# Kernel optimization log

Hardware: AMD Instinct MI355X
Metric: run time of the kernel (lower is better)

The kernel has to match this reference:

```python
import jax, jax.numpy as jnp
import numpy as np

BN_EPS = 1e-5

def _conv(x, W, b, stride, pad):
    # x: [B,C,H,W], W: [O,I,kh,kw]
    y = jax.lax.conv_general_dilated(
        x, W, window_strides=(stride, stride),
        padding=[(pad, pad), (pad, pad)],
        dimension_numbers=('NCHW', 'OIHW', 'NCHW'))
    return y + b[None, :, None, None]

def _bn(x, gamma, beta, mean, var):
    inv = gamma * jax.lax.rsqrt(var + BN_EPS)
    return x * inv[None, :, None, None] + (beta - mean * inv)[None, :, None, None]

def _haar_cD(x):
    # pywt.dwt2(x, 'haar') diagonal detail over last two axes (even H,W):
    # cD[i,j] = (x[2i,2j] - x[2i,2j+1] - x[2i+1,2j] + x[2i+1,2j+1]) / 2
    a = x[..., 0::2, 0::2]
    b = x[..., 0::2, 1::2]
    c = x[..., 1::2, 0::2]
    d = x[..., 1::2, 1::2]
    return (a - b - c + d) * 0.5

def setup_inputs() -> dict:
    key = jax.random.key(0)
    ks = jax.random.split(key, 20)
    B = 8192
    f32 = jnp.float32
    inp = {
        'x':   jax.random.normal(ks[0], (B, 3, 32, 32), dtype=f32),
        # conv1: 3 -> 32, k5 s2 p2
        'w1':  jax.random.normal(ks[1], (32, 3, 5, 5), dtype=f32) * 0.05,
        'b1':  jnp.zeros((32,), f32),
        'g1':  jnp.ones((32,), f32),
        'be1': jnp.zeros((32,), f32),
        'm1':  jax.random.normal(ks[2], (32,), dtype=f32) * 0.1,
        'v1':  jax.random.uniform(ks[3], (32,), dtype=f32, minval=0.5, maxval=1.5),
        # conv2: 32 -> 64, k3 s2 p1
        'w2':  jax.random.normal(ks[4], (64, 32, 3, 3), dtype=f32) * 0.05,
        'b2':  jnp.zeros((64,), f32),
        'g2':  jnp.ones((64,), f32),
        'be2': jnp.zeros((64,), f32),
        'm2':  jax.random.normal(ks[5], (64,), dtype=f32) * 0.1,
        'v2':  jax.random.uniform(ks[6], (64,), dtype=f32, minval=0.5, maxval=1.5),
        # attention conv: 64 -> 1, k1
        'wa':  jax.random.normal(ks[7], (1, 64, 1, 1), dtype=f32) * 0.1,
        'ba':  jnp.zeros((1,), f32),
        # decoder linears (torch Linear layout: [out, in])
        'wd1': jax.random.normal(ks[8], (512, 64 * 8 * 8), dtype=f32) * 0.02,
        'bd1': jnp.zeros((512,), f32),
        'wd2': jax.random.normal(ks[9], (128, 512), dtype=f32) * 0.04,
        'bd2': jnp.zeros((128,), f32),
    }
    return inp

def reference(x, w1, b1, g1, be1, m1, v1, w2, b2, g2, be2, m2, v2,
              wa, ba, wd1, bd1, wd2, bd2):
    # wavelet_conv stem
    h = jax.nn.relu(_bn(_conv(x, w1, b1, 2, 2), g1, be1, m1, v1))   # [B,32,16,16]
    feat = jax.nn.relu(_bn(_conv(h, w2, b2, 2, 1), g2, be2, m2, v2))  # [B,64,8,8]
    # Haar DWT diagonal-detail gate (detached in the original)
    cD = jax.lax.stop_gradient(_haar_cD(feat))                        # [B,64,4,4]
    cD_up = jnp.repeat(jnp.repeat(cD, 2, axis=-2), 2, axis=-1)        # [B,64,8,8]
    feat = feat * cD_up
    # attention gate
    attn = jax.nn.sigmoid(_conv(feat, wa, ba, 1, 0))                  # [B,1,8,8]
    feat = feat * attn
    # decode
    f = feat.reshape(feat.shape[0], -1)                               # [B,4096]
    h1 = jax.nn.relu(f @ wd1.T + bd1)                                  # [B,512]
    return jax.nn.sigmoid(h1 @ wd2.T + bd2)                            # [B,128]
```

## Files before the change

kernel.cpp:

```cpp
#include <hip/hip_runtime.h>
#include <hip/hip_bf16.h>

typedef __bf16 bf16x8 __attribute__((ext_vector_type(8)));
typedef __bf16 bf16x4 __attribute__((ext_vector_type(4)));
typedef float f32x4 __attribute__((ext_vector_type(4)));

#define BN_EPS 1e-5f

__device__ __forceinline__ void gl_lds16(const __bf16* g, __bf16* l) {
    __builtin_amdgcn_global_load_lds(
        (const __attribute__((address_space(1))) unsigned int*)g,
        (__attribute__((address_space(3))) unsigned int*)l,
        16, 0, 0);
}

__global__ __launch_bounds__(256) void wd1p_kernel(const float* __restrict__ wd1, __bf16* __restrict__ o) {
    __shared__ float t2[64][65];
    const int n = blockIdx.x;
    const int tid = threadIdx.x;
    const float* src = wd1 + (size_t)n * 4096;
    #pragma unroll
    for (int r = 0; r < 16; ++r) {
        int j = r * 256 + tid;
        t2[j & 63][j >> 6] = src[j];
    }
    __syncthreads();
    __bf16* dst = o + (size_t)n * 4096;
    #pragma unroll
    for (int r = 0; r < 16; ++r) {
        int t = r * 256 + tid;
        dst[t] = (__bf16)t2[t >> 6][t & 63];
    }
}

__global__ void prep_kernel(const float* __restrict__ wd2, const float* __restrict__ w1,
                            const float* __restrict__ w2,
                            __bf16* __restrict__ wd2o, __bf16* __restrict__ w1o,
                            __bf16* __restrict__ w2o) {
    int i = blockIdx.x * 256 + threadIdx.x;
    if (i < 65536) { wd2o[i] = (__bf16)wd2[i]; return; }
    i -= 65536;
    if (i < 4096) {
        int oc = i >> 7, rem = i & 127;
        int ot = rem >> 3, j = rem & 7;
        float v = 0.f;
        if (ot < 15 && j < 5) {
            int ic = ot / 5, ky = ot % 5;
            v = w1[((oc * 3 + ic) * 5 + ky) * 5 + j];
        }
        w1o[i] = (__bf16)v;
        return;
    }
    i -= 4096;
    if (i < 18432) {
        int oc = i / 288, rem = i % 288;
        int tap = rem / 32, ic = rem % 32;
        w2o[i] = (__bf16)w2[(oc * 32 + ic) * 9 + tap];
    }
}

__global__ __launch_bounds__(256, 5) void conv_fused_kernel(
    const float* __restrict__ x,
    const __bf16* __restrict__ w1r, const float* __restrict__ b1,
    const float* __restrict__ g1, const float* __restrict__ be1,
    const float* __restrict__ m1, const float* __restrict__ v1,
    const __bf16* __restrict__ w2r, const float* __restrict__ b2,
    const float* __restrict__ g2, const float* __restrict__ be2,
    const float* __restrict__ m2, const float* __restrict__ v2,
    const float* __restrict__ wa, const float* __restrict__ ba,
    __bf16* __restrict__ f)
{
    __shared__ __align__(16) __bf16 xsb[3 * 36 * 40];
    __shared__ __align__(16) char  ubuf[23120];
    __bf16* hsf  = (__bf16*)ubuf;
    float*  feat = (float*)ubuf;
    float*  cds  = (float*)(ubuf + 16384);
    float*  atn  = (float*)(ubuf + 20480);

    const int b    = blockIdx.x;
    const int tid  = threadIdx.x;
    const int lane = tid & 63;
    const int wave = tid >> 6;
    const int lo   = lane >> 4;
    const int ln   = lane & 15;

    {
        bf16x8 z = {};
        for (int i = tid; i < 540; i += 256) *(bf16x8*)&xsb[i * 8] = z;
        if (tid < 132) {
            int pi = tid >> 2, ch = tid & 3;
            int pix = (pi < 17) ? pi : (pi - 16) * 17;
            *(bf16x8*)&hsf[pix * 40 + ch * 8] = z;
        }
    }
    __syncthreads();

    {
        const float4* xb = (const float4*)(x + (size_t)b * 3072);
        #pragma unroll
        for (int r = 0; r < 3; ++r) {
            int c = r * 256 + tid;
            int plane = c >> 8, rem = c & 255;
            int row = rem >> 3, c4 = rem & 7;
            float4 v = xb[c];
            bf16x4 h;
            h[0] = (__bf16)v.x; h[1] = (__bf16)v.y; h[2] = (__bf16)v.z; h[3] = (__bf16)v.w;
            *(bf16x4*)&xsb[plane * 1440 + (row + 2) * 40 + 4 + c4 * 4] = h;
        }
    }

    bf16x8 bw1[2][4];
    #pragma unroll
    for (int nt = 0; nt < 2; ++nt)
        #pragma unroll
        for (int s = 0; s < 4; ++s)
            bw1[nt][s] = *(const bf16x8*)(w1r + (nt * 16 + ln) * 128 + (s * 4 + lo) * 8);
    __syncthreads();

    f32x4 c1[4][2] = {};
    const unsigned int* xw = (const unsigned int*)xsb;
    #pragma unroll
    for (int s = 0; s < 4; ++s) {
        const int o  = s * 4 + lo;
        const int ic = (o * 205) >> 10;
        const int ky = o - ic * 5;
        const bool dummy = (o == 15);
        const int icc = dummy ? 2 : ic;
        #pragma unroll
        for (int mt = 0; mt < 4; ++mt) {
            const int oy  = wave * 4 + mt;
            const int row = dummy ? 35 : (2 * oy + ky);
            const int dw  = icc * 720 + row * 20 + ln + 1;
            union { unsigned int u[4]; bf16x8 v; } fa;
            fa.u[0] = xw[dw]; fa.u[1] = xw[dw + 1]; fa.u[2] = xw[dw + 2]; fa.u[3] = 0;
            #pragma unroll
            for (int nt = 0; nt < 2; ++nt)
                c1[mt][nt] = __builtin_amdgcn_mfma_f32_16x16x32_bf16(fa.v, bw1[nt][s], c1[mt][nt], 0, 0, 0);
        }
    }

    #pragma unroll
    for (int nt = 0; nt < 2; ++nt) {
        const int oc  = nt * 16 + ln;
        const float inv = g1[oc] * rsqrtf(v1[oc] + BN_EPS);
        const float bb  = be1[oc] + (b1[oc] - m1[oc]) * inv;
        #pragma unroll
        for (int mt = 0; mt < 4; ++mt) {
            const int hy = wave * 4 + mt + 1;
            #pragma unroll
            for (int r = 0; r < 4; ++r) {
                const int hx = lo * 4 + r + 1;
                hsf[(hy * 17 + hx) * 40 + oc] = (__bf16)fmaxf(c1[mt][nt][r] * inv + bb, 0.f);
            }
        }
    }

    const int wm = wave >> 1, wn = wave & 1;
    bf16x8 bw2[2][9];
    #pragma unroll
    for (int nt = 0; nt < 2; ++nt) {
        const __bf16* wp = w2r + (wn * 32 + nt * 16 + ln) * 288 + lo * 8;
        #pragma unroll
        for (int ks = 0; ks < 9; ++ks)
            bw2[nt][ks] = *(const bf16x8*)(wp + ks * 32);
    }
    __syncthreads();

    f32x4 c2[2][2] = {};
    {
        int pixbase[2];
        #pragma unroll
        for (int mt = 0; mt < 2; ++mt) {
            int p = wm * 32 + mt * 16 + ln;
            int qy = p >> 3, qx = p & 7;
            pixbase[mt] = (2 * qy * 17 + 2 * qx) * 40 + lo * 8;
        }
        #pragma unroll
        for (int ks = 0; ks < 9; ++ks) {
            const int ty = ks / 3, tx = ks % 3;
            bf16x8 af[2];
            #pragma unroll
            for (int mt = 0; mt < 2; ++mt)
                af[mt] = *(const bf16x8*)&hsf[pixbase[mt] + (ty * 17 + tx) * 40];
            #pragma unroll
            for (int mt = 0; mt < 2; ++mt)
                #pragma unroll
                for (int nt = 0; nt < 2; ++nt)
                    c2[mt][nt] = __builtin_amdgcn_mfma_f32_16x16x32_bf16(af[mt], bw2[nt][ks], c2[mt][nt], 0, 0, 0);
        }
    }
    __syncthreads();

    #pragma unroll
    for (int nt = 0; nt < 2; ++nt) {
        const int oc  = wn * 32 + nt * 16 + ln;
        const float inv = g2[oc] * rsqrtf(v2[oc] + BN_EPS);
        const float bb  = be2[oc] + (b2[oc] - m2[oc]) * inv;
        #pragma unroll
        for (int mt = 0; mt < 2; ++mt)
            #pragma unroll
            for (int r = 0; r < 4; ++r) {
                const int p = wm * 32 + mt * 16 + lo * 4 + r;
                feat[oc * 64 + p] = fmaxf(c2[mt][nt][r] * inv + bb, 0.f);
            }
    }
    __syncthreads();

    #pragma unroll
    for (int r = 0; r < 4; ++r) {
        int idx = tid * 4 + r;
        int c = idx >> 4, yx = idx & 15;
        int y = yx >> 2, xx = yx & 3;
        float aa = feat[c * 64 + (2 * y) * 8 + 2 * xx];
        float bb = feat[c * 64 + (2 * y) * 8 + 2 * xx + 1];
        float cc = feat[c * 64 + (2 * y + 1) * 8 + 2 * xx];
        float dd = feat[c * 64 + (2 * y + 1) * 8 + 2 * xx + 1];
        cds[c * 16 + yx] = 0.5f * (aa - bb - cc + dd);
    }
    __syncthreads();

    const int q  = tid & 63;
    const int g  = wave;
    const int qy2 = q >> 3, qx2 = q & 7;
    const int qq = (qy2 >> 1) * 4 + (qx2 >> 1);
    float a2[16];
    float part = 0.f;
    #pragma unroll
    for (int j = 0; j < 16; ++j) {
        int oc = g * 16 + j;
        float v = feat[oc * 64 + q] * cds[oc * 16 + qq];
        a2[j] = v;
        part += v * wa[oc];
    }
    atn[g * 64 + q] = part;
    __syncthreads();
    float s2  = atn[q] + atn[64 + q] + atn[128 + q] + atn[192 + q] + ba[0];
    float sig = 1.f / (1.f + __expf(-s2));

    bf16x8 fo0, fo1;
    #pragma unroll
    for (int j = 0; j < 8; ++j) {
        fo0[j] = (__bf16)(a2[j] * sig);
        fo1[j] = (__bf16)(a2[j + 8] * sig);
    }
    __bf16* fb = f + (size_t)b * 4096 + q * 64 + g * 16;
    *(bf16x8*)fb = fo0;
    *(bf16x8*)(fb + 8) = fo1;
}

__global__ __launch_bounds__(256) void gemm1_kernel(
    const __bf16* __restrict__ A, const __bf16* __restrict__ B,
    const float* __restrict__ bias, __bf16* __restrict__ C)
{
    const int K = 4096, NOUT = 512;
    __shared__ __align__(16) __bf16 As[64][64];
    __shared__ __align__(16) __bf16 Bs[128][64];
    const int tid  = threadIdx.x;
    const int lane = tid & 63;
    const int wave = tid >> 6;
    const int lo = lane >> 4, ln = lane & 15;
    const int m0 = blockIdx.x * 64, n0 = blockIdx.y * 128;
    const int sw = ln & 7;
    f32x4 acc[4][2] = {};
    for (int k0 = 0; k0 < K; k0 += 64) {
        #pragma unroll
        for (int r = 0; r < 2; ++r) {
            int i = r * 256 + tid;
            int row = i >> 3, cs = i & 7;
            gl_lds16(A + (size_t)(m0 + row) * K + k0 + (cs ^ (row & 7)) * 8, &As[0][0] + i * 8);
        }
        #pragma unroll
        for (int r = 0; r < 4; ++r) {
            int i = r * 256 + tid;
            int row = i >> 3, cs = i & 7;
            gl_lds16(B + (size_t)(n0 + row) * K + k0 + (cs ^ (row & 7)) * 8, &Bs[0][0] + i * 8);
        }
        __syncthreads();
        #pragma unroll
        for (int s = 0; s < 2; ++s) {
            const int c = s * 4 + lo;
            const int slot = (c ^ sw) * 8;
            bf16x8 af[4], bfr[2];
            #pragma unroll
            for (int mt = 0; mt < 4; ++mt)
                af[mt] = *(const bf16x8*)(&As[mt * 16 + ln][slot]);
            #pragma unroll
            for (int nt = 0; nt < 2; ++nt)
                bfr[nt] = *(const bf16x8*)(&Bs[wave * 32 + nt * 16 + ln][slot]);
            #pragma unroll
            for (int mt = 0; mt < 4; ++mt)
                #pragma unroll
                for (int nt = 0; nt < 2; ++nt)
                    acc[mt][nt] = __builtin_amdgcn_mfma_f32_16x16x32_bf16(af[mt], bfr[nt], acc[mt][nt], 0, 0, 0);
        }
        __syncthreads();
    }
    #pragma unroll
    for (int mt = 0; mt < 4; ++mt)
        #pragma unroll
        for (int nt = 0; nt < 2; ++nt)
            #pragma unroll
            for (int r = 0; r < 4; ++r) {
                int m = m0 + mt * 16 + lo * 4 + r;
                int n = n0 + wave * 32 + nt * 16 + ln;
                float v = acc[mt][nt][r] + bias[n];
                C[(size_t)m * NOUT + n] = (__bf16)fmaxf(v, 0.f);
            }
}

__global__ __launch_bounds__(256) void gemm2_kernel(
    const __bf16* __restrict__ A, const __bf16* __restrict__ B,
    const float* __restrict__ bias, float* __restrict__ Out)
{
    const int K = 512, NOUT = 128;
    __shared__ __align__(16) __bf16 As[64][64];
    __shared__ __align__(16) __bf16 Bs[128][64];
    const int tid  = threadIdx.x;
    const int lane = tid & 63;
    const int wave = tid >> 6;
    const int lo = lane >> 4, ln = lane & 15;
    const int m0 = blockIdx.x * 64;
    const int sw = ln & 7;
    f32x4 acc[4][2] = {};
    for (int k0 = 0; k0 < K; k0 += 64) {
        #pragma unroll
        for (int r = 0; r < 2; ++r) {
            int i = r * 256 + tid;
            int row = i >> 3, cs = i & 7;
            gl_lds16(A + (size_t)(m0 + row) * K + k0 + (cs ^ (row & 7)) * 8, &As[0][0] + i * 8);
        }
        #pragma unroll
        for (int r = 0; r < 4; ++r) {
            int i = r * 256 + tid;
            int row = i >> 3, cs = i & 7;
            gl_lds16(B + (size_t)row * K + k0 + (cs ^ (row & 7)) * 8, &Bs[0][0] + i * 8);
        }
        __syncthreads();
        #pragma unroll
        for (int s = 0; s < 2; ++s) {
            const int c = s * 4 + lo;
            const int slot = (c ^ sw) * 8;
            bf16x8 af[4], bfr[2];
            #pragma unroll
            for (int mt = 0; mt < 4; ++mt)
                af[mt] = *(const bf16x8*)(&As[mt * 16 + ln][slot]);
            #pragma unroll
            for (int nt = 0; nt < 2; ++nt)
                bfr[nt] = *(const bf16x8*)(&Bs[wave * 32 + nt * 16 + ln][slot]);
            #pragma unroll
            for (int mt = 0; mt < 4; ++mt)
                #pragma unroll
                for (int nt = 0; nt < 2; ++nt)
                    acc[mt][nt] = __builtin_amdgcn_mfma_f32_16x16x32_bf16(af[mt], bfr[nt], acc[mt][nt], 0, 0, 0);
        }
        __syncthreads();
    }
    #pragma unroll
    for (int mt = 0; mt < 4; ++mt)
        #pragma unroll
        for (int nt = 0; nt < 2; ++nt)
            #pragma unroll
            for (int r = 0; r < 4; ++r) {
                int m = m0 + mt * 16 + lo * 4 + r;
                int n = wave * 32 + nt * 16 + ln;
                float v = acc[mt][nt][r] + bias[n];
                Out[(size_t)m * NOUT + n] = 1.f / (1.f + __expf(-v));
            }
}

extern "C" void kernel_launch(void* const* d_in, const int* in_sizes, int n_in,
                              void* d_out, int out_size, void* d_ws, size_t ws_size,
                              hipStream_t stream)
{
    const float* x   = (const float*)d_in[0];
    const float* w1  = (const float*)d_in[1];
    const float* b1  = (const float*)d_in[2];
    const float* g1  = (const float*)d_in[3];
    const float* be1 = (const float*)d_in[4];
    const float* m1  = (const float*)d_in[5];
    const float* v1  = (const float*)d_in[6];
    const float* w2  = (const float*)d_in[7];
    const float* b2  = (const float*)d_in[8];
    const float* g2  = (const float*)d_in[9];
    const float* be2 = (const float*)d_in[10];
    const float* m2  = (const float*)d_in[11];
    const float* v2  = (const float*)d_in[12];
    const float* wa  = (const float*)d_in[13];
    const float* ba  = (const float*)d_in[14];
    const float* wd1 = (const float*)d_in[15];
    const float* bd1 = (const float*)d_in[16];
    const float* wd2 = (const float*)d_in[17];
    const float* bd2 = (const float*)d_in[18];

    char* ws = (char*)d_ws;
    __bf16* f_bf   = (__bf16*)(ws);
    __bf16* h1_bf  = (__bf16*)(ws + 67108864);
    __bf16* wd1_bf = (__bf16*)(ws + 67108864 + 8388608);
    __bf16* wd2_bf = (__bf16*)(ws + 67108864 + 8388608 + 4194304);
    __bf16* w2r_bf = (__bf16*)(ws + 67108864 + 8388608 + 4194304 + 131072);
    __bf16* w1r_bf = (__bf16*)(ws + 67108864 + 8388608 + 4194304 + 131072 + 65536);

    prep_kernel<<<344, 256, 0, stream>>>(wd2, w1, w2, wd2_bf, w1r_bf, w2r_bf);
    wd1p_kernel<<<512, 256, 0, stream>>>(wd1, wd1_bf);

    conv_fused_kernel<<<8192, 256, 0, stream>>>(x, w1r_bf, b1, g1, be1, m1, v1,
                                                w2r_bf, b2, g2, be2, m2, v2, wa, ba, f_bf);

    dim3 g3(128, 4);
    gemm1_kernel<<<g3, 256, 0, stream>>>(f_bf, wd1_bf, bd1, h1_bf);

    gemm2_kernel<<<128, 256, 0, stream>>>(h1_bf, wd2_bf, bd2, (float*)d_out);
}
```

Measured before the change: 314.9 us.

## Transpose conv MFMA operands for vectorized epilogues; enlarge gemm1 tile to 128x128

The conv kernel swaps the MFMA operand order so each lane holds four consecutive output channels. That allows vectorized BN parameter loads, bf16x4 stores of conv1 output, and float4 stores of conv2 features into a new pixel-major, XOR-swizzled LDS layout, with matching vectorized reads in the Haar and attention stages. The aim is to cut scalar LDS traffic and bank conflicts. gemm1 now uses 128x128 tiles with a 2x2 wave layout and half as many M blocks. This raises reuse per block but doubles the accumulator registers and cuts the grid size.

```diff
diff --git a/kernel.cpp b/kernel.cpp
--- a/kernel.cpp
+++ b/kernel.cpp
@@ -57,6 +57,10 @@
         int tap = rem / 32, ic = rem % 32;
         w2o[i] = (__bf16)w2[(oc * 32 + ic) * 9 + tap];
     }
+}
+
+__device__ __forceinline__ int feat_addr(int p, int c) {
+    return p * 68 + ((((c >> 2) ^ ((p >> 3) & 3)) << 2) | (c & 3));
 }
 
 __global__ __launch_bounds__(256, 5) void conv_fused_kernel(
@@ -74,8 +78,8 @@
     __shared__ __align__(16) char  ubuf[23120];
     __bf16* hsf  = (__bf16*)ubuf;
     float*  feat = (float*)ubuf;
-    float*  cds  = (float*)(ubuf + 16384);
-    float*  atn  = (float*)(ubuf + 20480);
+    float*  cds  = (float*)(ubuf + 17408);
+    float*  atn  = (float*)(ubuf + 21760);
 
     const int b    = blockIdx.x;
     const int tid  = threadIdx.x;
@@ -111,10 +115,10 @@
 
     bf16x8 bw1[2][4];
     #pragma unroll
-    for (int nt = 0; nt < 2; ++nt)
+    for (int oct = 0; oct < 2; ++oct)
         #pragma unroll
         for (int s = 0; s < 4; ++s)
-            bw1[nt][s] = *(const bf16x8*)(w1r + (nt * 16 + ln) * 128 + (s * 4 + lo) * 8);
+            bw1[oct][s] = *(const bf16x8*)(w1r + (oct * 16 + ln) * 128 + (s * 4 + lo) * 8);
     __syncthreads();
 
     f32x4 c1[4][2] = {};
@@ -134,35 +138,44 @@
             union { unsigned int u[4]; bf16x8 v; } fa;
             fa.u[0] = xw[dw]; fa.u[1] = xw[dw + 1]; fa.u[2] = xw[dw + 2]; fa.u[3] = 0;
             #pragma unroll
-            for (int nt = 0; nt < 2; ++nt)
-                c1[mt][nt] = __builtin_amdgcn_mfma_f32_16x16x32_bf16(fa.v, bw1[nt][s], c1[mt][nt], 0, 0, 0);
-        }
-    }
-
-    #pragma unroll
-    for (int nt = 0; nt < 2; ++nt) {
-        const int oc  = nt * 16 + ln;
-        const float inv = g1[oc] * rsqrtf(v1[oc] + BN_EPS);
-        const float bb  = be1[oc] + (b1[oc] - m1[oc]) * inv;
+            for (int oct = 0; oct < 2; ++oct)
+                c1[mt][oct] = __builtin_amdgcn_mfma_f32_16x16x32_bf16(bw1[oct][s], fa.v, c1[mt][oct], 0, 0, 0);
+        }
+    }
+
+    #pragma unroll
+    for (int oct = 0; oct < 2; ++oct) {
+        const int ocb = oct * 16 + lo * 4;
+        const float4 gv = *(const float4*)(g1 + ocb);
+        const float4 vv = *(const float4*)(v1 + ocb);
+        const float4 bev = *(const float4*)(be1 + ocb);
+        const float4 b1v = *(const float4*)(b1 + ocb);
+        const float4 mv = *(const float4*)(m1 + ocb);
+        float inv[4], bb[4];
+        inv[0] = gv.x * rsqrtf(vv.x + BN_EPS); bb[0] = bev.x + (b1v.x - mv.x) * inv[0];
+        inv[1] = gv.y * rsqrtf(vv.y + BN_EPS); bb[1] = bev.y + (b1v.y - mv.y) * inv[1];
+        inv[2] = gv.z * rsqrtf(vv.z + BN_EPS); bb[2] = bev.z + (b1v.z - mv.z) * inv[2];
+        inv[3] = gv.w * rsqrtf(vv.w + BN_EPS); bb[3] = bev.w + (b1v.w - mv.w) * inv[3];
         #pragma unroll
         for (int mt = 0; mt < 4; ++mt) {
             const int hy = wave * 4 + mt + 1;
-            #pragma unroll
-            for (int r = 0; r < 4; ++r) {
-                const int hx = lo * 4 + r + 1;
-                hsf[(hy * 17 + hx) * 40 + oc] = (__bf16)fmaxf(c1[mt][nt][r] * inv + bb, 0.f);
-            }
+            const int hx = ln + 1;
+            bf16x4 hv;
+            #pragma unroll
+            for (int r = 0; r < 4; ++r)
+                hv[r] = (__bf16)fmaxf(c1[mt][oct][r] * inv[r] + bb[r], 0.f);
+            *(bf16x4*)&hsf[(hy * 17 + hx) * 40 + ocb] = hv;
         }
     }
 
     const int wm = wave >> 1, wn = wave & 1;
     bf16x8 bw2[2][9];
     #pragma unroll
-    for (int nt = 0; nt < 2; ++nt) {
-        const __bf16* wp = w2r + (wn * 32 + nt * 16 + ln) * 288 + lo * 8;
+    for (int oct = 0; oct < 2; ++oct) {
+        const __bf16* wp = w2r + (wn * 32 + oct * 16 + ln) * 288 + lo * 8;
         #pragma unroll
         for (int ks = 0; ks < 9; ++ks)
-            bw2[nt][ks] = *(const bf16x8*)(wp + ks * 32);
+            bw2[oct][ks] = *(const bf16x8*)(wp + ks * 32);
     }
     __syncthreads();
 
@@ -170,39 +183,50 @@
     {
         int pixbase[2];
         #pragma unroll
-        for (int mt = 0; mt < 2; ++mt) {
-            int p = wm * 32 + mt * 16 + ln;
+        for (int np = 0; np < 2; ++np) {
+            int p = wm * 32 + np * 16 + ln;
             int qy = p >> 3, qx = p & 7;
-            pixbase[mt] = (2 * qy * 17 + 2 * qx) * 40 + lo * 8;
+            pixbase[np] = (2 * qy * 17 + 2 * qx) * 40 + lo * 8;
         }
         #pragma unroll
         for (int ks = 0; ks < 9; ++ks) {
             const int ty = ks / 3, tx = ks % 3;
-            bf16x8 af[2];
-            #pragma unroll
-            for (int mt = 0; mt < 2; ++mt)
-                af[mt] = *(const bf16x8*)&hsf[pixbase[mt] + (ty * 17 + tx) * 40];
-            #pragma unroll
-            for (int mt = 0; mt < 2; ++mt)
+            bf16x8 bfp[2];
+            #pragma unroll
+            for (int np = 0; np < 2; ++np)
+                bfp[np] = *(const bf16x8*)&hsf[pixbase[np] + (ty * 17 + tx) * 40];
+            #pragma unroll
+            for (int oct = 0; oct < 2; ++oct)
                 #pragma unroll
-                for (int nt = 0; nt < 2; ++nt)
-                    c2[mt][nt] = __builtin_amdgcn_mfma_f32_16x16x32_bf16(af[mt], bw2[nt][ks], c2[mt][nt], 0, 0, 0);
-        }
-    }
-    __syncthreads();
-
-    #pragma unroll
-    for (int nt = 0; nt < 2; ++nt) {
-        const int oc  = wn * 32 + nt * 16 + ln;
-        const float inv = g2[oc] * rsqrtf(v2[oc] + BN_EPS);
-        const float bb  = be2[oc] + (b2[oc] - m2[oc]) * inv;
-        #pragma unroll
-        for (int mt = 0; mt < 2; ++mt)
-            #pragma unroll
-            for (int r = 0; r < 4; ++r) {
-                const int p = wm * 32 + mt * 16 + lo * 4 + r;
-                feat[oc * 64 + p] = fmaxf(c2[mt][nt][r] * inv + bb, 0.f);
-            }
+                for (int np = 0; np < 2; ++np)
+                    c2[oct][np] = __builtin_amdgcn_mfma_f32_16x16x32_bf16(bw2[oct][ks], bfp[np], c2[oct][np], 0, 0, 0);
+        }
+    }
+    __syncthreads();
+
+    #pragma unroll
+    for (int oct = 0; oct < 2; ++oct) {
+        const int ocb = wn * 32 + oct * 16 + lo * 4;
+        const float4 gv = *(const float4*)(g2 + ocb);
+        const float4 vv = *(const float4*)(v2 + ocb);
+        const float4 bev = *(const float4*)(be2 + ocb);
+        const float4 b2v = *(const float4*)(b2 + ocb);
+        const float4 mv = *(const float4*)(m2 + ocb);
+        float inv[4], bb[4];
+        inv[0] = gv.x * rsqrtf(vv.x + BN_EPS); bb[0] = bev.x + (b2v.x - mv.x) * inv[0];
+        inv[1] = gv.y * rsqrtf(vv.y + BN_EPS); bb[1] = bev.y + (b2v.y - mv.y) * inv[1];
+        inv[2] = gv.z * rsqrtf(vv.z + BN_EPS); bb[2] = bev.z + (b2v.z - mv.z) * inv[2];
+        inv[3] = gv.w * rsqrtf(vv.w + BN_EPS); bb[3] = bev.w + (b2v.w - mv.w) * inv[3];
+        const int j = ocb >> 2;
+        #pragma unroll
+        for (int np = 0; np < 2; ++np) {
+            const int p = wm * 32 + np * 16 + ln;
+            f32x4 out;
+            #pragma unroll
+            for (int r = 0; r < 4; ++r)
+                out[r] = fmaxf(c2[oct][np][r] * inv[r] + bb[r], 0.f);
+            *(f32x4*)&feat[p * 68 + ((j ^ ((p >> 3) & 3)) << 2)] = out;
+        }
     }
     __syncthreads();
 
@@ -211,11 +235,12 @@
         int idx = tid * 4 + r;
         int c = idx >> 4, yx = idx & 15;
         int y = yx >> 2, xx = yx & 3;
-        float aa = feat[c * 64 + (2 * y) * 8 + 2 * xx];
-        float bb = feat[c * 64 + (2 * y) * 8 + 2 * xx + 1];
-        float cc = feat[c * 64 + (2 * y + 1) * 8 + 2 * xx];
-        float dd = feat[c * 64 + (2 * y + 1) * 8 + 2 * xx + 1];
-        cds[c * 16 + yx] = 0.5f * (aa - bb - cc + dd);
+        int p00 = 16 * y + 2 * xx;
+        float aa = feat[feat_addr(p00, c)];
+        float bb = feat[feat_addr(p00 + 1, c)];
+        float cc = feat[feat_addr(p00 + 8, c)];
+        float dd = feat[feat_addr(p00 + 9, c)];
+        cds[yx * 68 + c] = 0.5f * (aa - bb - cc + dd);
     }
     __syncthreads();
 
@@ -226,11 +251,14 @@
     float a2[16];
     float part = 0.f;
     #pragma unroll
-    for (int j = 0; j < 16; ++j) {
-        int oc = g * 16 + j;
-        float v = feat[oc * 64 + q] * cds[oc * 16 + qq];
-        a2[j] = v;
-        part += v * wa[oc];
+    for (int jj = 0; jj < 4; ++jj) {
+        const int j = g * 4 + jj;
+        f32x4 fv = *(const f32x4*)&feat[q * 68 + ((j ^ ((q >> 3) & 3)) << 2)];
+        f32x4 cv = *(const f32x4*)&cds[qq * 68 + j * 4];
+        const float4 wv = *(const float4*)(wa + j * 4);
+        float v0 = fv[0] * cv[0], v1x = fv[1] * cv[1], v2x = fv[2] * cv[2], v3 = fv[3] * cv[3];
+        a2[jj * 4 + 0] = v0; a2[jj * 4 + 1] = v1x; a2[jj * 4 + 2] = v2x; a2[jj * 4 + 3] = v3;
+        part += v0 * wv.x + v1x * wv.y + v2x * wv.z + v3 * wv.w;
     }
     atn[g * 64 + q] = part;
     __syncthreads();
@@ -253,18 +281,19 @@
     const float* __restrict__ bias, __bf16* __restrict__ C)
 {
     const int K = 4096, NOUT = 512;
-    __shared__ __align__(16) __bf16 As[64][64];
+    __shared__ __align__(16) __bf16 As[128][64];
     __shared__ __align__(16) __bf16 Bs[128][64];
     const int tid  = threadIdx.x;
     const int lane = tid & 63;
     const int wave = tid >> 6;
+    const int wm = wave >> 1, wn = wave & 1;
     const int lo = lane >> 4, ln = lane & 15;
-    const int m0 = blockIdx.x * 64, n0 = blockIdx.y * 128;
+    const int m0 = blockIdx.x * 128, n0 = blockIdx.y * 128;
     const int sw = ln & 7;
-    f32x4 acc[4][2] = {};
+    f32x4 acc[4][4] = {};
     for (int k0 = 0; k0 < K; k0 += 64) {
         #pragma unroll
-        for (int r = 0; r < 2; ++r) {
+        for (int r = 0; r < 4; ++r) {
             int i = r * 256 + tid;
             int row = i >> 3, cs = i & 7;
             gl_lds16(A + (size_t)(m0 + row) * K + k0 + (cs ^ (row & 7)) * 8, &As[0][0] + i * 8);
@@ -280,30 +309,33 @@
         for (int s = 0; s < 2; ++s) {
             const int c = s * 4 + lo;
             const int slot = (c ^ sw) * 8;
-            bf16x8 af[4], bfr[2];
+            bf16x8 af[4], bfr[4];
             #pragma unroll
             for (int mt = 0; mt < 4; ++mt)
-                af[mt] = *(const bf16x8*)(&As[mt * 16 + ln][slot]);
-            #pragma unroll
-            for (int nt = 0; nt < 2; ++nt)
-                bfr[nt] = *(const bf16x8*)(&Bs[wave * 32 + nt * 16 + ln][slot]);
+                af[mt] = *(const bf16x8*)(&As[wm * 64 + mt * 16 + ln][slot]);
+            #pragma unroll
+            for (int nt = 0; nt < 4; ++nt)
+                bfr[nt] = *(const bf16x8*)(&Bs[wn * 64 + nt * 16 + ln][slot]);
             #pragma unroll
             for (int mt = 0; mt < 4; ++mt)
                 #pragma unroll
-                for (int nt = 0; nt < 2; ++nt)
+                for (int nt = 0; nt < 4; ++nt)
                     acc[mt][nt] = __builtin_amdgcn_mfma_f32_16x16x32_bf16(af[mt], bfr[nt], acc[mt][nt], 0, 0, 0);
         }
         __syncthreads();
     }
+    float bv[4];
+    #pragma unroll
+    for (int nt = 0; nt < 4; ++nt) bv[nt] = bias[n0 + wn * 64 + nt * 16 + ln];
     #pragma unroll
     for (int mt = 0; mt < 4; ++mt)
         #pragma unroll
-        for (int nt = 0; nt < 2; ++nt)
+        for (int nt = 0; nt < 4; ++nt)
             #pragma unroll
             for (int r = 0; r < 4; ++r) {
-                int m = m0 + mt * 16 + lo * 4 + r;
-                int n = n0 + wave * 32 + nt * 16 + ln;
-                float v = acc[mt][nt][r] + bias[n];
+                int m = m0 + wm * 64 + mt * 16 + lo * 4 + r;
+                int n = n0 + wn * 64 + nt * 16 + ln;
+                float v = acc[mt][nt][r] + bv[nt];
                 C[(size_t)m * NOUT + n] = (__bf16)fmaxf(v, 0.f);
             }
 }
@@ -406,7 +438,7 @@
     conv_fused_kernel<<<8192, 256, 0, stream>>>(x, w1r_bf, b1, g1, be1, m1, v1,
                                                 w2r_bf, b2, g2, be2, m2, v2, wa, ba, f_bf);
 
-    dim3 g3(128, 4);
+    dim3 g3(64, 4);
     gemm1_kernel<<<g3, 256, 0, stream>>>(f_bf, wd1_bf, bd1, h1_bf);
 
     gemm2_kernel<<<128, 256, 0, stream>>>(h1_bf, wd2_bf, bd2, (float*)d_out);
```

New measurement: 352.9 us. +12.1%, slower.

## Split-K the first decoder GEMM and halve gemm2 row tiles for more blocks

Applied to the files above, without the earlier changes.

The first decoder GEMM is split along K into two halves, launched as a 3D grid that doubles the block count from 512 to 1024. Each half writes fp32 partial sums to a new workspace buffer, and a separate reduce kernel adds them with bias, applies ReLU and converts to bf16. gemm2 drops to 32-row tiles so it launches 256 blocks instead of 128, and it gains an occupancy hint. The aim is to fill the GPU's compute units better, at the cost of 32MB of extra fp32 partial traffic plus one more kernel launch. The split path runs only when the workspace is large enough, otherwise it falls back to the original GEMM.

```diff
diff --git a/kernel.cpp b/kernel.cpp
--- a/kernel.cpp
+++ b/kernel.cpp
@@ -248,6 +248,82 @@
     *(bf16x8*)(fb + 8) = fo1;
 }
 
+__global__ __launch_bounds__(256, 4) void gemm1_split_kernel(
+    const __bf16* __restrict__ A, const __bf16* __restrict__ B,
+    float* __restrict__ P)
+{
+    const int K = 4096, NOUT = 512, KH = 2048;
+    __shared__ __align__(16) __bf16 As[64][64];
+    __shared__ __align__(16) __bf16 Bs[128][64];
+    const int tid  = threadIdx.x;
+    const int lane = tid & 63;
+    const int wave = tid >> 6;
+    const int lo = lane >> 4, ln = lane & 15;
+    const int m0 = blockIdx.x * 64, n0 = blockIdx.y * 128;
+    const int ks0 = blockIdx.z * KH;
+    const int sw = ln & 7;
+    f32x4 acc[4][2] = {};
+    for (int k0 = ks0; k0 < ks0 + KH; k0 += 64) {
+        #pragma unroll
+        for (int r = 0; r < 2; ++r) {
+            int i = r * 256 + tid;
+            int row = i >> 3, cs = i & 7;
+            gl_lds16(A + (size_t)(m0 + row) * K + k0 + (cs ^ (row & 7)) * 8, &As[0][0] + i * 8);
+        }
+        #pragma unroll
+        for (int r = 0; r < 4; ++r) {
+            int i = r * 256 + tid;
+            int row = i >> 3, cs = i & 7;
+            gl_lds16(B + (size_t)(n0 + row) * K + k0 + (cs ^ (row & 7)) * 8, &Bs[0][0] + i * 8);
+        }
+        __syncthreads();
+        #pragma unroll
+        for (int s = 0; s < 2; ++s) {
+            const int c = s * 4 + lo;
+            const int slot = (c ^ sw) * 8;
+            bf16x8 af[4], bfr[2];
+            #pragma unroll
+            for (int mt = 0; mt < 4; ++mt)
+                af[mt] = *(const bf16x8*)(&As[mt * 16 + ln][slot]);
+            #pragma unroll
+            for (int nt = 0; nt < 2; ++nt)
+                bfr[nt] = *(const bf16x8*)(&Bs[wave * 32 + nt * 16 + ln][slot]);
+            #pragma unroll
+            for (int mt = 0; mt < 4; ++mt)
+                #pragma unroll
+                for (int nt = 0; nt < 2; ++nt)
+                    acc[mt][nt] = __builtin_amdgcn_mfma_f32_16x16x32_bf16(af[mt], bfr[nt], acc[mt][nt], 0, 0, 0);
+        }
+        __syncthreads();
+    }
+    float* Pp = P + (size_t)blockIdx.z * 8192 * 512;
+    #pragma unroll
+    for (int mt = 0; mt < 4; ++mt)
+        #pragma unroll
+        for (int nt = 0; nt < 2; ++nt)
+            #pragma unroll
+            for (int r = 0; r < 4; ++r) {
+                int m = m0 + mt * 16 + lo * 4 + r;
+                int n = n0 + wave * 32 + nt * 16 + ln;
+                Pp[(size_t)m * NOUT + n] = acc[mt][nt][r];
+            }
+}
+
+__global__ __launch_bounds__(256) void reduce1_kernel(
+    const float* __restrict__ P, const float* __restrict__ bias, __bf16* __restrict__ h1)
+{
+    const size_t HALF = (size_t)8192 * 512;
+    size_t i4 = ((size_t)blockIdx.x * 256 + threadIdx.x) * 4;
+    f32x4 p0 = *(const f32x4*)(P + i4);
+    f32x4 p1 = *(const f32x4*)(P + HALF + i4);
+    f32x4 bv = *(const f32x4*)(bias + (i4 & 511));
+    bf16x4 o;
+    #pragma unroll
+    for (int j = 0; j < 4; ++j)
+        o[j] = (__bf16)fmaxf(p0[j] + p1[j] + bv[j], 0.f);
+    *(bf16x4*)(h1 + i4) = o;
+}
+
 __global__ __launch_bounds__(256) void gemm1_kernel(
     const __bf16* __restrict__ A, const __bf16* __restrict__ B,
     const float* __restrict__ bias, __bf16* __restrict__ C)
@@ -308,24 +384,23 @@
             }
 }
 
-__global__ __launch_bounds__(256) void gemm2_kernel(
+__global__ __launch_bounds__(256, 4) void gemm2_kernel(
     const __bf16* __restrict__ A, const __bf16* __restrict__ B,
     const float* __restrict__ bias, float* __restrict__ Out)
 {
     const int K = 512, NOUT = 128;
-    __shared__ __align__(16) __bf16 As[64][64];
+    __shared__ __align__(16) __bf16 As[32][64];
     __shared__ __align__(16) __bf16 Bs[128][64];
     const int tid  = threadIdx.x;
     const int lane = tid & 63;
     const int wave = tid >> 6;
     const int lo = lane >> 4, ln = lane & 15;
-    const int m0 = blockIdx.x * 64;
+    const int m0 = blockIdx.x * 32;
     const int sw = ln & 7;
-    f32x4 acc[4][2] = {};
+    f32x4 acc[2][2] = {};
     for (int k0 = 0; k0 < K; k0 += 64) {
-        #pragma unroll
-        for (int r = 0; r < 2; ++r) {
-            int i = r * 256 + tid;
+        {
+            int i = tid;
             int row = i >> 3, cs = i & 7;
             gl_lds16(A + (size_t)(m0 + row) * K + k0 + (cs ^ (row & 7)) * 8, &As[0][0] + i * 8);
         }
@@ -340,15 +415,15 @@
         for (int s = 0; s < 2; ++s) {
             const int c = s * 4 + lo;
             const int slot = (c ^ sw) * 8;
-            bf16x8 af[4], bfr[2];
-            #pragma unroll
-            for (int mt = 0; mt < 4; ++mt)
+            bf16x8 af[2], bfr[2];
+            #pragma unroll
+            for (int mt = 0; mt < 2; ++mt)
                 af[mt] = *(const bf16x8*)(&As[mt * 16 + ln][slot]);
             #pragma unroll
             for (int nt = 0; nt < 2; ++nt)
                 bfr[nt] = *(const bf16x8*)(&Bs[wave * 32 + nt * 16 + ln][slot]);
             #pragma unroll
-            for (int mt = 0; mt < 4; ++mt)
+            for (int mt = 0; mt < 2; ++mt)
                 #pragma unroll
                 for (int nt = 0; nt < 2; ++nt)
                     acc[mt][nt] = __builtin_amdgcn_mfma_f32_16x16x32_bf16(af[mt], bfr[nt], acc[mt][nt], 0, 0, 0);
@@ -356,7 +431,7 @@
         __syncthreads();
     }
     #pragma unroll
-    for (int mt = 0; mt < 4; ++mt)
+    for (int mt = 0; mt < 2; ++mt)
         #pragma unroll
         for (int nt = 0; nt < 2; ++nt)
             #pragma unroll
@@ -393,12 +468,28 @@
     const float* bd2 = (const float*)d_in[18];
 
     char* ws = (char*)d_ws;
-    __bf16* f_bf   = (__bf16*)(ws);
-    __bf16* h1_bf  = (__bf16*)(ws + 67108864);
-    __bf16* wd1_bf = (__bf16*)(ws + 67108864 + 8388608);
-    __bf16* wd2_bf = (__bf16*)(ws + 67108864 + 8388608 + 4194304);
-    __bf16* w2r_bf = (__bf16*)(ws + 67108864 + 8388608 + 4194304 + 131072);
-    __bf16* w1r_bf = (__bf16*)(ws + 67108864 + 8388608 + 4194304 + 131072 + 65536);
+    const size_t SZ_F  = 67108864;
+    const size_t SZ_P  = 33554432;
+    const size_t SZ_H1 = 8388608;
+    const bool use_split = ws_size >= (SZ_F + SZ_P + SZ_H1 + 4194304 + 131072 + 65536 + 8192);
+
+    __bf16* f_bf = (__bf16*)ws;
+    float*  P;
+    __bf16* h1_bf;
+    char* tail;
+    if (use_split) {
+        P      = (float*)(ws + SZ_F);
+        h1_bf  = (__bf16*)(ws + SZ_F + SZ_P);
+        tail   = ws + SZ_F + SZ_P + SZ_H1;
+    } else {
+        P      = nullptr;
+        h1_bf  = (__bf16*)(ws + SZ_F);
+        tail   = ws + SZ_F + SZ_H1;
+    }
+    __bf16* wd1_bf = (__bf16*)tail;
+    __bf16* wd2_bf = (__bf16*)(tail + 4194304);
+    __bf16* w2r_bf = (__bf16*)(tail + 4194304 + 131072);
+    __bf16* w1r_bf = (__bf16*)(tail + 4194304 + 131072 + 65536);
 
     prep_kernel<<<344, 256, 0, stream>>>(wd2, w1, w2, wd2_bf, w1r_bf, w2r_bf);
     wd1p_kernel<<<512, 256, 0, stream>>>(wd1, wd1_bf);
@@ -406,8 +497,14 @@
     conv_fused_kernel<<<8192, 256, 0, stream>>>(x, w1r_bf, b1, g1, be1, m1, v1,
                                                 w2r_bf, b2, g2, be2, m2, v2, wa, ba, f_bf);
 
-    dim3 g3(128, 4);
-    gemm1_kernel<<<g3, 256, 0, stream>>>(f_bf, wd1_bf, bd1, h1_bf);
-
-    gemm2_kernel<<<128, 256, 0, stream>>>(h1_bf, wd2_bf, bd2, (float*)d_out);
-}
+    if (use_split) {
+        dim3 g3(128, 4, 2);
+        gemm1_split_kernel<<<g3, 256, 0, stream>>>(f_bf, wd1_bf, P);
+        reduce1_kernel<<<4096, 256, 0, stream>>>(P, bd1, h1_bf);
+    } else {
+        dim3 g3(128, 4);
+        gemm1_kernel<<<g3, 256, 0, stream>>>(f_bf, wd1_bf, bd1, h1_bf);
+    }
+
+    gemm2_kernel<<<256, 256, 0, stream>>>(h1_bf, wd2_bf, bd2, (float*)d_out);
+}
```

Result: faster. 307.4 us (-2.4%).
